# Optimization experiments

Measured on AMD Instinct MI355X. Metric: run time of the kernel, lower is better.

## Reference

```python
import jax, jax.numpy as jnp
import numpy as np

N, L, E, H, D = 4, 2048, 1024, 16, 64

def setup_inputs() -> dict:
    key = jax.random.key(0)
    ks = jax.random.split(key, 8)
    s = 1.0 / np.sqrt(E)
    return {
        "Q": jax.random.normal(ks[0], (N, L, E), jnp.float32),
        "K": jax.random.normal(ks[1], (N, L, E), jnp.float32),
        "V": jax.random.normal(ks[2], (N, L, E), jnp.float32),
        "Wq": jax.random.normal(ks[3], (H * D, E), jnp.float32) * s,
        "bq": jnp.zeros((H * D,), jnp.float32),
        "Wk": jax.random.normal(ks[4], (H * D, E), jnp.float32) * s,
        "bk": jnp.zeros((H * D,), jnp.float32),
        "Wv": jax.random.normal(ks[5], (H * D, E), jnp.float32) * s,
        "bv": jnp.zeros((H * D,), jnp.float32),
        "Wo": jax.random.normal(ks[6], (E, H * D), jnp.float32) * s,
        "bo": jnp.zeros((E,), jnp.float32),
    }

def reference(Q, K, V, Wq, bq, Wk, bk, Wv, bv, Wo, bo):
    n, lq, e = Q.shape
    lk = K.shape[1]
    # projections: Linear(x) = x @ W.T + b
    q = (Q @ Wq.T + bq).reshape(n, lq, H, D)
    k = (K @ Wk.T + bk).reshape(n, lk, H, D)
    v = (V @ Wv.T + bv).reshape(n, lk, H, D)
    # scores over key dim (original broadcasts Q*K and sums over d)
    scores = jnp.einsum('nqhd,nkhd->nqkh', q, k) / jnp.sqrt(jnp.float32(D))
    attn = jax.nn.softmax(scores, axis=2)  # softmax over key axis
    out = jnp.einsum('nqkh,nkhd->nqhd', attn, v)
    out = out.reshape(n, lq, H * D)
    return (out @ Wo.T + bo).reshape(n, lq, E)
```

## Files before the change

### kernel.cpp

```cpp
#include <hip/hip_runtime.h>
#include <cstdint>
#include <cstddef>


typedef __bf16 bf16x8 __attribute__((ext_vector_type(8)));
typedef __bf16 bf16x4 __attribute__((ext_vector_type(4)));
typedef __bf16 bf16x2 __attribute__((ext_vector_type(2)));
typedef float f32x4 __attribute__((ext_vector_type(4)));
typedef float f32x2 __attribute__((ext_vector_type(2)));
typedef unsigned int uint2v __attribute__((ext_vector_type(2)));
typedef unsigned int uint4v __attribute__((ext_vector_type(4)));

#define LOG2E_OVER_SQRTD 0.18033688011112042f

__device__ __forceinline__ unsigned short f2bf(float f) {
  unsigned int u = __builtin_bit_cast(unsigned int, f);
  u = (u + 0x7fffu + ((u >> 16) & 1u)) >> 16;
  return (unsigned short)u;
}

__device__ __forceinline__ unsigned int pk2(float a, float b) {
  f32x2 t = {a, b};
  bf16x2 h = __builtin_convertvector(t, bf16x2);
  return __builtin_bit_cast(unsigned int, h);
}

__device__ __forceinline__ void gl2lds16(const void* g, void* l) {
  __builtin_amdgcn_global_load_lds(
      (__attribute__((address_space(1))) unsigned int*)g,
      (__attribute__((address_space(3))) unsigned int*)l, 16, 0, 0);
}

__device__ __forceinline__ bf16x8 mk_ap(f32x4 sA, f32x4 sB) {
  float peA[4], peB[4];
#pragma unroll
  for (int r = 0; r < 4; ++r) {
    peA[r] = __builtin_amdgcn_exp2f(sA[r]);
    peB[r] = __builtin_amdgcn_exp2f(sB[r]);
  }
  unsigned int x00 = pk2(peA[0], peA[1]);
  unsigned int x01 = pk2(peA[2], peA[3]);
  unsigned int x10 = pk2(peB[0], peB[1]);
  unsigned int x11 = pk2(peB[2], peB[3]);
  uint2v s0 = __builtin_amdgcn_permlane32_swap(x00, x10, false, false);
  uint2v t0 = __builtin_amdgcn_permlane16_swap(s0[0], s0[1], false, false);
  uint2v s1 = __builtin_amdgcn_permlane32_swap(x01, x11, false, false);
  uint2v t1 = __builtin_amdgcn_permlane16_swap(s1[0], s1[1], false, false);
  uint4v u;
  u[0] = t0[0];
  u[1] = t1[0];
  u[2] = t0[1];
  u[3] = t1[1];
  return __builtin_bit_cast(bf16x8, u);
}

struct CvtArgs {
  const float* src[7];
  unsigned short* dst[7];
};
__global__ __launch_bounds__(256) void cvt_all_k(CvtArgs a) {
  int bid = blockIdx.x;
  int which, x;
  if (bid < 24576) {
    which = bid >> 13;
    x = bid & 8191;
  } else {
    int r = bid - 24576;
    which = 3 + (r >> 10);
    x = r & 1023;
  }
  const float* s = a.src[which];
  unsigned short* d = a.dst[which];
  size_t i = ((size_t)x * 256 + threadIdx.x) * 4;
  float4 v = *(const float4*)(s + i);
  ushort4 o;
  o.x = f2bf(v.x); o.y = f2bf(v.y); o.z = f2bf(v.z); o.w = f2bf(v.w);
  *(ushort4*)(d + i) = o;
}

struct GemmDesc {
  const unsigned short* A;
  const unsigned short* Bt;
  const float* bias;
  void* C;
  int N;
  int nbx_shift;
  float scale;
  int bias_row;
  int permc;
};
struct GemmPack3 {
  GemmDesc g[3];
};

template <bool OUT_F32>
__global__ __launch_bounds__(256, 2) void gemm_multi_k(GemmPack3 p) {
  __shared__ __attribute__((aligned(16))) unsigned short As[128 * 64];
  __shared__ __attribute__((aligned(16))) unsigned short Bs[128 * 64];
  const GemmDesc d = p.g[blockIdx.x >> 9];
  int t = blockIdx.x & 511;
  if (d.nbx_shift == 3) t = ((t & 7) << 6) | (t >> 3);
  const int bx = t & ((1 << d.nbx_shift) - 1);
  const int by = t >> d.nbx_shift;

  const int tid = threadIdx.x;
  const int lane = tid & 63, wave = tid >> 6;
  const int lr = lane & 15, lg = lane >> 4;
  const int rowBase = by * 128;
  const int colBase = bx * 128;
  const int wm = (wave & 1) * 64, wn = (wave >> 1) * 64;

  f32x4 acc[4][4] = {};

  const unsigned short* gA[4];
  const unsigned short* gB[4];
  unsigned short* lA[4];
  unsigned short* lB[4];
#pragma unroll
  for (int i = 0; i < 4; ++i) {
    int s = tid + i * 256;
    int row = s >> 3;
    int c = (s & 7) ^ (row & 7);
    gA[i] = d.A + (size_t)(rowBase + row) * 1024 + c * 8;
    gB[i] = d.Bt + (size_t)(colBase + row) * 1024 + c * 8;
    lA[i] = &As[s * 8];
    lB[i] = &Bs[s * 8];
  }

  for (int kt = 0; kt < 16; ++kt) {
    const int ko = kt * 64;
#pragma unroll
    for (int i = 0; i < 4; ++i) {
      gl2lds16(gA[i] + ko, lA[i]);
      gl2lds16(gB[i] + ko, lB[i]);
    }
    __syncthreads();

#pragma unroll
    for (int ks = 0; ks < 2; ++ks) {
      bf16x8 af[4], bfr[4];
#pragma unroll
      for (int mt = 0; mt < 4; ++mt) {
        int row = wm + mt * 16 + lr;
        int c = (ks * 4 + lg) ^ (row & 7);
        af[mt] = *(const bf16x8*)&As[row * 64 + c * 8];
      }
#pragma unroll
      for (int nt = 0; nt < 4; ++nt) {
        int row = wn + nt * 16 + lr;
        int c = (ks * 4 + lg) ^ (row & 7);
        bfr[nt] = *(const bf16x8*)&Bs[row * 64 + c * 8];
      }
#pragma unroll
      for (int mt = 0; mt < 4; ++mt)
#pragma unroll
        for (int nt = 0; nt < 4; ++nt)
          acc[mt][nt] = __builtin_amdgcn_mfma_f32_16x16x32_bf16(
              af[mt], bfr[nt], acc[mt][nt], 0, 0, 0);
    }
    __syncthreads();
  }

#pragma unroll
  for (int mt = 0; mt < 4; ++mt)
#pragma unroll
    for (int nt = 0; nt < 4; ++nt) {
      int col = colBase + wn + nt * 16 + lr;
      int colStore = d.permc ? (colBase + wn + lr * 4 + nt) : col;
      float bcol = d.bias_row ? 0.f : d.bias[col];
#pragma unroll
      for (int r = 0; r < 4; ++r) {
        int row = rowBase + wm + mt * 16 + lg * 4 + r;
        float b = d.bias_row ? d.bias[row] : bcol;
        float val = (acc[mt][nt][r] + b) * d.scale;
        size_t idx = (size_t)row * (size_t)d.N + (size_t)colStore;
        if (OUT_F32)
          ((float*)d.C)[idx] = val;
        else
          ((unsigned short*)d.C)[idx] = f2bf(val);
      }
    }
}

__global__ __launch_bounds__(256, 4) void attn_k(
    const unsigned short* __restrict__ qb,
    const unsigned short* __restrict__ kb,
    const unsigned short* __restrict__ vtb,
    unsigned short* __restrict__ aob) {
  __shared__ __attribute__((aligned(16))) unsigned short Ks[2 * 64 * 64];
  __shared__ __attribute__((aligned(16))) unsigned short Vts[2 * 64 * 64];

  const int tid = threadIdx.x;
  const int lane = tid & 63, wave = tid >> 6;
  const int lr = lane & 15, lg = lane >> 4;

  const int bid = blockIdx.x;
  const int xcd = bid & 7;
  const int idx = bid >> 3;
  const int qt = idx & 15;
  const int nh = (idx >> 4) * 8 + xcd;
  const int h = nh & 15, n = nh >> 4;
  const int q0 = qt * 128;

#pragma unroll
  for (int i = 0; i < 4; ++i) {
    int s = i * 256 + tid;
    int row = s >> 3;
    int c = (s & 7) ^ (row & 7);
    gl2lds16(qb + (((size_t)n * 2048 + q0 + row) << 10) + h * 64 + c * 8,
             &Ks[s * 8]);
  }
  __syncthreads();

  bf16x8 aq[2][2];
#pragma unroll
  for (int mt = 0; mt < 2; ++mt)
#pragma unroll
    for (int ks = 0; ks < 2; ++ks) {
      int row = wave * 32 + mt * 16 + lr;
      int c = (ks * 4 + lg) ^ (row & 7);
      aq[mt][ks] = *(const bf16x8*)&Ks[row * 64 + c * 8];
    }
  __syncthreads();

  const int a0 = lr * 64 + ((lg ^ (lr & 7)) * 8);
  const int a1 = lr * 64 + (((4 + lg) ^ (lr & 7)) * 8);
  const unsigned short* Kb0 = &Ks[a0];
  const unsigned short* Kb1 = &Ks[a1];
  const unsigned short* Vb0 = &Vts[a0];
  const unsigned short* Vb1 = &Vts[a1];

  const unsigned short* kg[2];
  const unsigned short* vg[2];
  int ldo[2];
#pragma unroll
  for (int i = 0; i < 2; ++i) {
    int s = i * 256 + tid;
    int row = s >> 3;
    int c = (s & 7) ^ (row & 7);
    kg[i] = kb + (((size_t)n * 2048 + row) << 10) + h * 64 + c * 8;
    vg[i] = vtb + (((size_t)(h * 64 + row)) << 13) + (size_t)n * 2048 + c * 8;
    ldo[i] = s * 8;
  }
#pragma unroll
  for (int i = 0; i < 2; ++i) {
    gl2lds16(kg[i], &Ks[ldo[i]]);
    gl2lds16(vg[i], &Vts[ldo[i]]);
    kg[i] += 64 * 1024;
    vg[i] += 64;
  }

  bf16x8 ones;
#pragma unroll
  for (int i = 0; i < 8; ++i) ones[i] = (__bf16)1.0f;
  const f32x4 fzero = {0.f, 0.f, 0.f, 0.f};

  f32x4 o_acc[2][4] = {};
  f32x4 o_sum[2] = {};

#pragma unroll 2
  for (int kt = 0; kt < 32; ++kt) {
    const int cb = (kt & 1) * 4096;
    const int nb = 4096 - cb;
    __syncthreads();

    if (kt < 31) {
#pragma unroll
      for (int i = 0; i < 2; ++i) {
        gl2lds16(kg[i], &Ks[nb + ldo[i]]);
        gl2lds16(vg[i], &Vts[nb + ldo[i]]);
        kg[i] += 64 * 1024;
        vg[i] += 64;
      }
    }

    f32x4 sA[2][2], sB[2][2];
    {
      bf16x8 k00 = *(const bf16x8*)(Kb0 + cb);
      bf16x8 k10 = *(const bf16x8*)(Kb1 + cb);
      bf16x8 k01 = *(const bf16x8*)(Kb0 + cb + 1024);
      bf16x8 k11 = *(const bf16x8*)(Kb1 + cb + 1024);
      __builtin_amdgcn_s_setprio(1);
#pragma unroll
      for (int mt = 0; mt < 2; ++mt) {
        f32x4 t0 = __builtin_amdgcn_mfma_f32_16x16x32_bf16(
            k00, aq[mt][0], fzero, 0, 0, 0);
        sA[mt][0] = __builtin_amdgcn_mfma_f32_16x16x32_bf16(
            k10, aq[mt][1], t0, 0, 0, 0);
        f32x4 t1 = __builtin_amdgcn_mfma_f32_16x16x32_bf16(
            k01, aq[mt][0], fzero, 0, 0, 0);
        sA[mt][1] = __builtin_amdgcn_mfma_f32_16x16x32_bf16(
            k11, aq[mt][1], t1, 0, 0, 0);
      }
      __builtin_amdgcn_s_setprio(0);
    }
    {
      bf16x8 k02 = *(const bf16x8*)(Kb0 + cb + 2048);
      bf16x8 k12 = *(const bf16x8*)(Kb1 + cb + 2048);
      bf16x8 k03 = *(const bf16x8*)(Kb0 + cb + 3072);
      bf16x8 k13 = *(const bf16x8*)(Kb1 + cb + 3072);
      __builtin_amdgcn_s_setprio(1);
#pragma unroll
      for (int mt = 0; mt < 2; ++mt) {
        f32x4 t0 = __builtin_amdgcn_mfma_f32_16x16x32_bf16(
            k02, aq[mt][0], fzero, 0, 0, 0);
        sB[mt][0] = __builtin_amdgcn_mfma_f32_16x16x32_bf16(
            k12, aq[mt][1], t0, 0, 0, 0);
        f32x4 t1 = __builtin_amdgcn_mfma_f32_16x16x32_bf16(
            k03, aq[mt][0], fzero, 0, 0, 0);
        sB[mt][1] = __builtin_amdgcn_mfma_f32_16x16x32_bf16(
            k13, aq[mt][1], t1, 0, 0, 0);
      }
      __builtin_amdgcn_s_setprio(0);
    }

    {
      bf16x8 bv0[4];
#pragma unroll
      for (int nt = 0; nt < 4; ++nt)
        bv0[nt] = *(const bf16x8*)(Vb0 + cb + nt * 1024);

      bf16x8 ap0[2];
#pragma unroll
      for (int mt = 0; mt < 2; ++mt) ap0[mt] = mk_ap(sA[mt][0], sA[mt][1]);

      __builtin_amdgcn_s_setprio(1);
#pragma unroll
      for (int mt = 0; mt < 2; ++mt) {
        o_sum[mt] = __builtin_amdgcn_mfma_f32_16x16x32_bf16(
            ap0[mt], ones, o_sum[mt], 0, 0, 0);
#pragma unroll
        for (int nt = 0; nt < 4; ++nt)
          o_acc[mt][nt] = __builtin_amdgcn_mfma_f32_16x16x32_bf16(
              ap0[mt], bv0[nt], o_acc[mt][nt], 0, 0, 0);
      }
      __builtin_amdgcn_s_setprio(0);
    }

    {
      bf16x8 bv1[4];
#pragma unroll
      for (int nt = 0; nt < 4; ++nt)
        bv1[nt] = *(const bf16x8*)(Vb1 + cb + nt * 1024);

      bf16x8 ap1[2];
#pragma unroll
      for (int mt = 0; mt < 2; ++mt) ap1[mt] = mk_ap(sB[mt][0], sB[mt][1]);

      __builtin_amdgcn_s_setprio(1);
#pragma unroll
      for (int mt = 0; mt < 2; ++mt) {
        o_sum[mt] = __builtin_amdgcn_mfma_f32_16x16x32_bf16(
            ap1[mt], ones, o_sum[mt], 0, 0, 0);
#pragma unroll
        for (int nt = 0; nt < 4; ++nt)
          o_acc[mt][nt] = __builtin_amdgcn_mfma_f32_16x16x32_bf16(
              ap1[mt], bv1[nt], o_acc[mt][nt], 0, 0, 0);
      }
      __builtin_amdgcn_s_setprio(0);
    }
  }

#pragma unroll
  for (int mt = 0; mt < 2; ++mt) {
#pragma unroll
    for (int r = 0; r < 4; ++r) {
      float inv = 1.0f / o_sum[mt][r];
      int row_l = q0 + wave * 32 + mt * 16 + lg * 4 + r;
      size_t base = (((size_t)n * 2048 + row_l) << 10) + h * 64;
#pragma unroll
      for (int nt = 0; nt < 4; ++nt)
        aob[base + nt * 16 + lr] = f2bf(o_acc[mt][nt][r] * inv);
    }
  }
}

extern "C" void kernel_launch(void* const* d_in, const int* in_sizes, int n_in,
                              void* d_out, int out_size, void* d_ws,
                              size_t ws_size, hipStream_t stream) {
  const float* Q = (const float*)d_in[0];
  const float* K = (const float*)d_in[1];
  const float* V = (const float*)d_in[2];
  const float* Wq = (const float*)d_in[3];
  const float* bq = (const float*)d_in[4];
  const float* Wk = (const float*)d_in[5];
  const float* bk = (const float*)d_in[6];
  const float* Wv = (const float*)d_in[7];
  const float* bv = (const float*)d_in[8];
  const float* Wo = (const float*)d_in[9];
  const float* bo = (const float*)d_in[10];

  const size_t S = (size_t)8192 * 1024;
  const size_t W = (size_t)1024 * 1024;
  unsigned short* ws = (unsigned short*)d_ws;
  unsigned short* Qbf = ws;
  unsigned short* Kbf = ws + S;
  unsigned short* Vbf = ws + 2 * S;
  unsigned short* qbuf = ws + 3 * S;
  unsigned short* kbuf = ws + 4 * S;
  unsigned short* vtbuf = ws + 5 * S;
  unsigned short* Wqb = ws + 6 * S;
  unsigned short* Wkb = Wqb + W;
  unsigned short* Wvb = Wqb + 2 * W;
  unsigned short* Wob = Wqb + 3 * W;
  unsigned short* aob = Qbf;

  CvtArgs cv;
  cv.src[0] = Q;  cv.dst[0] = Qbf;
  cv.src[1] = K;  cv.dst[1] = Kbf;
  cv.src[2] = V;  cv.dst[2] = Vbf;
  cv.src[3] = Wq; cv.dst[3] = Wqb;
  cv.src[4] = Wk; cv.dst[4] = Wkb;
  cv.src[5] = Wv; cv.dst[5] = Wvb;
  cv.src[6] = Wo; cv.dst[6] = Wob;
  cvt_all_k<<<28672, 256, 0, stream>>>(cv);

  GemmPack3 pp;
  pp.g[0] = {Qbf, Wqb, bq, qbuf, 1024, 3, LOG2E_OVER_SQRTD, 0, 0};
  pp.g[1] = {Kbf, Wkb, bk, kbuf, 1024, 3, 1.0f, 0, 0};
  pp.g[2] = {Wvb, Vbf, bv, vtbuf, 8192, 6, 1.0f, 1, 0};
  gemm_multi_k<false><<<1536, 256, 0, stream>>>(pp);

  attn_k<<<1024, 256, 0, stream>>>(qbuf, kbuf, vtbuf, aob);

  GemmPack3 po;
  po.g[0] = {aob, Wob, bo, d_out, 1024, 3, 1.0f, 0, 0};
  po.g[1] = po.g[0];
  po.g[2] = po.g[0];
  gemm_multi_k<true><<<512, 256, 0, stream>>>(po);
}
```

Baseline: 330.9 us.

## Double-buffer LDS tiles in projection GEMM to overlap loads with MFMA

The projection GEMM now keeps two LDS buffers for the A and B tiles. It issues the global-to-LDS loads for k-tile kt+1 right after the barrier, then runs MFMAs on tile kt, and drops the trailing barrier. This aims to hide global load latency behind matrix math and to cut one barrier per iteration. In exchange it doubles LDS use per block to 64KB, which can limit occupancy, and it depends on the async loads having completed by the next barrier.

```diff
diff --git a/kernel.cpp b/kernel.cpp
--- a/kernel.cpp
+++ b/kernel.cpp
@@ -95,8 +95,8 @@
 
 template <bool OUT_F32>
 __global__ __launch_bounds__(256, 2) void gemm_multi_k(GemmPack3 p) {
-  __shared__ __attribute__((aligned(16))) unsigned short As[128 * 64];
-  __shared__ __attribute__((aligned(16))) unsigned short Bs[128 * 64];
+  __shared__ __attribute__((aligned(16))) unsigned short As[2 * 128 * 64];
+  __shared__ __attribute__((aligned(16))) unsigned short Bs[2 * 128 * 64];
   const GemmDesc d = p.g[blockIdx.x >> 9];
   int t = blockIdx.x & 511;
   if (d.nbx_shift == 3) t = ((t & 7) << 6) | (t >> 3);
@@ -114,8 +114,7 @@
 
   const unsigned short* gA[4];
   const unsigned short* gB[4];
-  unsigned short* lA[4];
-  unsigned short* lB[4];
+  int so[4];
 #pragma unroll
   for (int i = 0; i < 4; ++i) {
     int s = tid + i * 256;
@@ -123,18 +122,28 @@
     int c = (s & 7) ^ (row & 7);
     gA[i] = d.A + (size_t)(rowBase + row) * 1024 + c * 8;
     gB[i] = d.Bt + (size_t)(colBase + row) * 1024 + c * 8;
-    lA[i] = &As[s * 8];
-    lB[i] = &Bs[s * 8];
+    so[i] = s * 8;
+  }
+
+#pragma unroll
+  for (int i = 0; i < 4; ++i) {
+    gl2lds16(gA[i], &As[so[i]]);
+    gl2lds16(gB[i], &Bs[so[i]]);
   }
 
   for (int kt = 0; kt < 16; ++kt) {
-    const int ko = kt * 64;
-#pragma unroll
-    for (int i = 0; i < 4; ++i) {
-      gl2lds16(gA[i] + ko, lA[i]);
-      gl2lds16(gB[i] + ko, lB[i]);
-    }
+    const int cb = (kt & 1) * 8192;
+    const int nb = 8192 - cb;
     __syncthreads();
+
+    if (kt < 15) {
+      const int ko = (kt + 1) * 64;
+#pragma unroll
+      for (int i = 0; i < 4; ++i) {
+        gl2lds16(gA[i] + ko, &As[nb + so[i]]);
+        gl2lds16(gB[i] + ko, &Bs[nb + so[i]]);
+      }
+    }
 
 #pragma unroll
     for (int ks = 0; ks < 2; ++ks) {
@@ -143,13 +152,13 @@
       for (int mt = 0; mt < 4; ++mt) {
         int row = wm + mt * 16 + lr;
         int c = (ks * 4 + lg) ^ (row & 7);
-        af[mt] = *(const bf16x8*)&As[row * 64 + c * 8];
+        af[mt] = *(const bf16x8*)&As[cb + row * 64 + c * 8];
       }
 #pragma unroll
       for (int nt = 0; nt < 4; ++nt) {
         int row = wn + nt * 16 + lr;
         int c = (ks * 4 + lg) ^ (row & 7);
-        bfr[nt] = *(const bf16x8*)&Bs[row * 64 + c * 8];
+        bfr[nt] = *(const bf16x8*)&Bs[cb + row * 64 + c * 8];
       }
 #pragma unroll
       for (int mt = 0; mt < 4; ++mt)
@@ -158,7 +167,6 @@
           acc[mt][nt] = __builtin_amdgcn_mfma_f32_16x16x32_bf16(
               af[mt], bfr[nt], acc[mt][nt], 0, 0, 0);
     }
-    __syncthreads();
   }
 
 #pragma unroll
```

Result: no change. 336.9 us (+1.8%).
